# Kernel optimization log

Hardware: AMD Instinct MI355X
Metric: run time of the kernel (lower is better)

The kernel has to match this reference:

```python
import jax, jax.numpy as jnp
import numpy as np

N = 50000      # num_users == num_products (required by the original forward's reuse of edge_index)
E = 800000
F_IN = 128
HID = 256
CLS = 64


def sage_conv(x_src, x_dst, e_src, e_dst, w_l, b_l, w_r, num_dst):
    """PyG SAGEConv (mean aggr, bipartite): lin_l(mean_j x_src[j]) + lin_r(x_dst)."""
    msg = x_src[e_src]                                             # [E, d]
    agg = jax.ops.segment_sum(msg, e_dst, num_segments=num_dst)    # [num_dst, d]
    cnt = jax.ops.segment_sum(jnp.ones((e_dst.shape[0],), x_src.dtype), e_dst,
                              num_segments=num_dst)
    mean = agg / jnp.maximum(cnt, 1.0)[:, None]
    return mean @ w_l.T + b_l + x_dst @ w_r.T


def setup_inputs() -> dict:
    key = jax.random.key(0)
    ks = jax.random.split(key, 16)
    def lin(k, out_d, in_d):
        s = 1.0 / np.sqrt(in_d)
        return jax.random.uniform(k, (out_d, in_d), jnp.float32, -s, s)
    return {
        'x_user': jax.random.normal(ks[0], (N, F_IN), jnp.float32),
        'x_product': jax.random.normal(ks[1], (N, F_IN), jnp.float32),
        'edge_index': jax.random.randint(ks[2], (2, E), 0, N, jnp.int64 if jax.config.jax_enable_x64 else jnp.int32),
        # user_conv1: (F_IN,F_IN)->HID
        'w_u1_l': lin(ks[3], HID, F_IN), 'b_u1': jnp.zeros((HID,), jnp.float32), 'w_u1_r': lin(ks[4], HID, F_IN),
        # product_conv1: (F_IN,F_IN)->HID
        'w_p1_l': lin(ks[5], HID, F_IN), 'b_p1': jnp.zeros((HID,), jnp.float32), 'w_p1_r': lin(ks[6], HID, F_IN),
        # user_conv2: (HID,HID)->CLS
        'w_u2_l': lin(ks[7], CLS, HID), 'b_u2': jnp.zeros((CLS,), jnp.float32), 'w_u2_r': lin(ks[8], CLS, HID),
        # product_conv2: (HID,HID)->CLS
        'w_p2_l': lin(ks[9], CLS, HID), 'b_p2': jnp.zeros((CLS,), jnp.float32), 'w_p2_r': lin(ks[10], CLS, HID),
    }


def reference(x_user, x_product, edge_index,
              w_u1_l, b_u1, w_u1_r, w_p1_l, b_p1, w_p1_r,
              w_u2_l, b_u2, w_u2_r, w_p2_l, b_p2, w_p2_r):
    u_idx, p_idx = edge_index[0], edge_index[1]
    # layer 1 (eval mode: dropout is identity)
    x_user_1 = jax.nn.relu(sage_conv(x_user, x_product, u_idx, p_idx,
                                     w_u1_l, b_u1, w_u1_r, N))        # [N, HID] (dst=product-sized)
    x_product_1 = jax.nn.relu(sage_conv(x_product, x_user, p_idx, u_idx,
                                        w_p1_l, b_p1, w_p1_r, N))     # [N, HID]
    # layer 2 (same edge_index reuse as the original code)
    x_user_2 = sage_conv(x_user_1, x_product_1, u_idx, p_idx,
                         w_u2_l, b_u2, w_u2_r, N)                     # [N, CLS]
    x_product_2 = sage_conv(x_product_1, x_user_1, p_idx, u_idx,
                            w_p2_l, b_p2, w_p2_r, N)                  # [N, CLS]
    return x_user_2, x_product_2
```

## Files before the change

### kernel.cpp

```cpp
#include <hip/hip_runtime.h>
#include <stdint.h>

#define Nn 50000
#define Ee 800000
#define FIN 128
#define HIDD 256
#define CLSS 64

#define NBIN 98
#define BSH 9
#define BINSZ 512
#define BCAP 16384
#define EPB 2048
#define NEB ((Ee + EPB - 1) / EPB)

#define MT_TOT 782
#define GX 112

typedef unsigned int uint_t;
typedef unsigned short us_t;
typedef __attribute__((ext_vector_type(8))) short short8;
typedef __attribute__((ext_vector_type(4))) float f32x4;
typedef __attribute__((ext_vector_type(2))) float f32x2;

__device__ inline float bflo(uint_t v) { union { uint_t u; float f; } c; c.u = v << 16; return c.f; }
__device__ inline float bfhi(uint_t v) { union { uint_t u; float f; } c; c.u = v & 0xffff0000u; return c.f; }
__device__ inline us_t f2bf(float f) {
    union { float f; uint_t u; } c; c.f = f;
    uint_t u = c.u;
    u += 0x7fffu + ((u >> 16) & 1u);
    return (us_t)(u >> 16);
}

#define GLOAD(gp, lp)                                                      \
    __builtin_amdgcn_global_load_lds(                                      \
        (const __attribute__((address_space(1))) unsigned int*)(gp),       \
        (__attribute__((address_space(3))) unsigned int*)(lp), 16, 0, 0)

__global__ __launch_bounds__(512) void k_front(
    const int* __restrict__ ei,
    const float* __restrict__ xu, const float* __restrict__ xp,
    const float* __restrict__ w1, const float* __restrict__ w2,
    const float* __restrict__ w3, const float* __restrict__ w4,
    const float* __restrict__ w5, const float* __restrict__ w6,
    const float* __restrict__ w7, const float* __restrict__ w8,
    us_t* __restrict__ cu, us_t* __restrict__ cp,
    uint_t* __restrict__ f8u, uint_t* __restrict__ f8p,
    us_t* __restrict__ wc10, us_t* __restrict__ wc11,
    us_t* __restrict__ wc20, us_t* __restrict__ wc21,
    int* __restrict__ bin_cnt,
    uint_t* __restrict__ ent_p, uint_t* __restrict__ ent_u) {
    __shared__ int hist[2 * NBIN];
    __shared__ int base[2 * NBIN];
    int bx = blockIdx.x, tid = threadIdx.x;

    if (bx < NEB) {
        int e0 = bx * EPB;
        int n = Ee - e0; if (n > EPB) n = EPB;
        for (int i = tid; i < 2 * NBIN; i += 512) hist[i] = 0;
        __syncthreads();
        for (int i = tid; i < n; i += 512) {
            int u = ei[e0 + i], p = ei[Ee + e0 + i];
            atomicAdd(&hist[p >> BSH], 1);
            atomicAdd(&hist[NBIN + (u >> BSH)], 1);
        }
        __syncthreads();
        for (int i = tid; i < 2 * NBIN; i += 512) {
            int c = hist[i];
            base[i] = c ? atomicAdd(&bin_cnt[i], c) : 0;
        }
        __syncthreads();
        for (int i = tid; i < 2 * NBIN; i += 512) hist[i] = base[i];
        __syncthreads();
        for (int i = tid; i < n; i += 512) {
            int u = ei[e0 + i], p = ei[Ee + e0 + i];
            int bp = p >> BSH, bu = u >> BSH;
            int rp = atomicAdd(&hist[bp], 1);
            if (rp < BCAP)
                ent_p[(size_t)bp * BCAP + rp] = ((uint_t)(p & (BINSZ - 1)) << 16) | (uint_t)u;
            int ru = atomicAdd(&hist[NBIN + bu], 1);
            if (ru < BCAP)
                ent_u[(size_t)bu * BCAP + ru] = ((uint_t)(u & (BINSZ - 1)) << 16) | (uint_t)p;
        }
    } else if (bx < NEB + 96) {
        int i = (bx - NEB) * 512 + tid;
        const float* wp; us_t* dst;
        if (i < 32768) {
            int seg = i >> 13; int loc = i & 8191;
            int row = loc >> 5, col = (loc & 31) * 4;
            switch (seg) {
                case 0: wp = w1; dst = wc10 + (size_t)row * 256 + col; break;
                case 1: wp = w2; dst = wc10 + (size_t)row * 256 + 128 + col; break;
                case 2: wp = w3; dst = wc11 + (size_t)row * 256 + col; break;
                default: wp = w4; dst = wc11 + (size_t)row * 256 + 128 + col; break;
            }
            float4 v = reinterpret_cast<const float4*>(wp)[i & 8191];
            ushort4 o;
            o.x = f2bf(v.x); o.y = f2bf(v.y); o.z = f2bf(v.z); o.w = f2bf(v.w);
            *reinterpret_cast<ushort4*>(dst) = o;
        } else {
            int j = i - 32768;
            int seg = j >> 12; int loc = j & 4095;
            switch (seg) {
                case 0: wp = w5; dst = wc20; break;
                case 1: wp = w6; dst = wc21 + 64 * 256; break;
                case 2: wp = w7; dst = wc21; break;
                default: wp = w8; dst = wc20 + 64 * 256; break;
            }
            float4 v = reinterpret_cast<const float4*>(wp)[loc];
            ushort4 o;
            o.x = f2bf(v.x); o.y = f2bf(v.y); o.z = f2bf(v.z); o.w = f2bf(v.w);
            reinterpret_cast<ushort4*>(dst)[loc] = o;
        }
    } else {
        int bcx = bx - NEB - 96;
        int side = bcx & 1;
        const float* in = side ? xp : xu;
        us_t* comb = side ? cu : cp;
        uint_t* o8 = side ? f8p : f8u;
        const int n4 = (Nn * FIN) / 4;
        int i = (bcx >> 1) * 512 + tid;
        int stride = 256 * 512;
        for (; i < n4; i += stride) {
            float4 v = reinterpret_cast<const float4*>(in)[i];
            ushort4 o;
            o.x = f2bf(v.x); o.y = f2bf(v.y); o.z = f2bf(v.z); o.w = f2bf(v.w);
            int node = i >> 5;
            int col = (i & 31) * 4;
            *reinterpret_cast<ushort4*>(comb + (size_t)node * 256 + 128 + col) = o;
            int pk = __builtin_amdgcn_cvt_pk_fp8_f32(v.x, v.y, 0, false);
            pk = __builtin_amdgcn_cvt_pk_fp8_f32(v.z, v.w, pk, true);
            o8[i] = (uint_t)pk;
        }
    }
}

__global__ __launch_bounds__(512) void k_scatter(
    const uint_t* __restrict__ ent_p, const uint_t* __restrict__ ent_u,
    const int* __restrict__ bin_cnt,
    int* __restrict__ off, int* __restrict__ cnt,
    int* __restrict__ src_p, int* __restrict__ src_u) {
    __shared__ int ca[BINSZ];
    __shared__ int cb[BINSZ];
    __shared__ int bb[128];
    int side = blockIdx.y, b = blockIdx.x, t = threadIdx.x;
    const uint_t* E = (side ? ent_u : ent_p) + (size_t)b * BCAP;
    int* src = side ? src_u : src_p;

    if (t < 128) {
        int v = 0;
        if (t < NBIN) { v = bin_cnt[side * NBIN + t]; if (v > BCAP) v = BCAP; }
        bb[t] = v;
    }
    __syncthreads();
    #pragma unroll
    for (int d = 1; d < 128; d <<= 1) {
        int x = 0;
        if (t < 128 && t >= d) x = bb[t - d];
        __syncthreads();
        if (t < 128) bb[t] += x;
        __syncthreads();
    }
    int nb = bin_cnt[side * NBIN + b]; if (nb > BCAP) nb = BCAP;
    int base = bb[b] - nb;

    ca[t] = 0;
    __syncthreads();
    for (int i = t; i < nb; i += 512)
        atomicAdd(&ca[E[i] >> 16], 1);
    __syncthreads();
    int v = ca[t];
    int* A = ca; int* B = cb;
    #pragma unroll
    for (int d = 1; d < BINSZ; d <<= 1) {
        int x = A[t] + ((t >= d) ? A[t - d] : 0);
        B[t] = x;
        __syncthreads();
        int* tmp = A; A = B; B = tmp;
    }
    int excl = A[t] - v;
    B[t] = excl;
    __syncthreads();
    for (int i = t; i < nb; i += 512) {
        uint_t e = E[i];
        int sl = atomicAdd(&B[e >> 16], 1);
        src[base + sl] = (int)(e & 0xffffu);
    }
    int d = (b << BSH) + t;
    if (d < Nn) {
        off[side * Nn + d] = base + excl;
        cnt[side * Nn + d] = v;
    }
}

__global__ __launch_bounds__(256) void k_agg1(
    const uint4* __restrict__ xu8, const uint4* __restrict__ xp8,
    const int* __restrict__ off, const int* __restrict__ cnt,
    const int* __restrict__ src_p, const int* __restrict__ src_u,
    us_t* __restrict__ cu, us_t* __restrict__ cp) {
    int side = blockIdx.y;
    const uint4* X = side ? xp8 : xu8;
    const int* of = off + side * Nn;
    const int* cn = cnt + side * Nn;
    const int* sr = side ? src_u : src_p;
    us_t* out = side ? cp : cu;

    int node = blockIdx.x * 32 + (threadIdx.x >> 3);
    if (node >= Nn) return;
    int l = threadIdx.x & 7;
    int s = of[node], c = cn[node];
    float ac[16];
    #pragma unroll
    for (int i = 0; i < 16; ++i) ac[i] = 0.f;

    int j = 0;
    for (; j + 8 <= c; j += 8) {
        int ss[8];
        #pragma unroll
        for (int q = 0; q < 8; ++q) ss[q] = sr[s + j + q];
        uint4 vv[8];
        #pragma unroll
        for (int q = 0; q < 8; ++q) vv[q] = X[(size_t)ss[q] * 8 + l];
        #pragma unroll
        for (int q = 0; q < 8; ++q) {
            const uint_t* pw = reinterpret_cast<const uint_t*>(&vv[q]);
            #pragma unroll
            for (int h = 0; h < 4; ++h) {
                f32x2 plo = __builtin_amdgcn_cvt_pk_f32_fp8((int)pw[h], false);
                f32x2 phi = __builtin_amdgcn_cvt_pk_f32_fp8((int)pw[h], true);
                ac[h * 4 + 0] += plo[0]; ac[h * 4 + 1] += plo[1];
                ac[h * 4 + 2] += phi[0]; ac[h * 4 + 3] += phi[1];
            }
        }
    }
    for (; j < c; ++j) {
        uint4 v0 = X[(size_t)sr[s + j] * 8 + l];
        const uint_t* pw = reinterpret_cast<const uint_t*>(&v0);
        #pragma unroll
        for (int h = 0; h < 4; ++h) {
            f32x2 plo = __builtin_amdgcn_cvt_pk_f32_fp8((int)pw[h], false);
            f32x2 phi = __builtin_amdgcn_cvt_pk_f32_fp8((int)pw[h], true);
            ac[h * 4 + 0] += plo[0]; ac[h * 4 + 1] += plo[1];
            ac[h * 4 + 2] += phi[0]; ac[h * 4 + 3] += phi[1];
        }
    }
    float inv = 1.0f / fmaxf((float)c, 1.0f);
    uint_t ow[8];
    #pragma unroll
    for (int i = 0; i < 8; ++i)
        ow[i] = (uint_t)f2bf(ac[2 * i] * inv) | ((uint_t)f2bf(ac[2 * i + 1] * inv) << 16);
    uint4* dst = reinterpret_cast<uint4*>(out + (size_t)node * 256 + l * 16);
    uint4 o0 = {ow[0], ow[1], ow[2], ow[3]};
    uint4 o1 = {ow[4], ow[5], ow[6], ow[7]};
    dst[0] = o0;
    dst[1] = o1;
}

__global__ __launch_bounds__(256) void k_agg2(
    const uint4* __restrict__ tu, const uint4* __restrict__ tp,
    const int* __restrict__ off, const int* __restrict__ cnt,
    const int* __restrict__ src_p, const int* __restrict__ src_u,
    float* __restrict__ ou, float* __restrict__ op) {
    int side = blockIdx.y;
    const uint4* T = side ? tp : tu;
    const int* of = off + side * Nn;
    const int* cn = cnt + side * Nn;
    const int* sr = side ? src_u : src_p;
    float* out = side ? op : ou;

    int node = blockIdx.x * 32 + (threadIdx.x >> 3);
    if (node >= Nn) return;
    int l = threadIdx.x & 7;
    int s = of[node], c = cn[node];
    float ac[8];
    #pragma unroll
    for (int i = 0; i < 8; ++i) ac[i] = 0.f;

    int j = 0;
    for (; j + 8 <= c; j += 8) {
        int ss[8];
        #pragma unroll
        for (int q = 0; q < 8; ++q) ss[q] = sr[s + j + q];
        uint4 vv[8];
        #pragma unroll
        for (int q = 0; q < 8; ++q) vv[q] = T[(size_t)ss[q] * 8 + l];
        #pragma unroll
        for (int q = 0; q < 8; ++q) {
            const uint_t* pw = reinterpret_cast<const uint_t*>(&vv[q]);
            #pragma unroll
            for (int h = 0; h < 4; ++h) {
                ac[h * 2 + 0] += bflo(pw[h]);
                ac[h * 2 + 1] += bfhi(pw[h]);
            }
        }
    }
    for (; j < c; ++j) {
        uint4 v0 = T[(size_t)sr[s + j] * 8 + l];
        const uint_t* pw = reinterpret_cast<const uint_t*>(&v0);
        #pragma unroll
        for (int h = 0; h < 4; ++h) {
            ac[h * 2 + 0] += bflo(pw[h]);
            ac[h * 2 + 1] += bfhi(pw[h]);
        }
    }
    float inv = 1.0f / fmaxf((float)c, 1.0f);
    float4* po = reinterpret_cast<float4*>(out + (size_t)node * 64) + l * 2;
    float4 p0 = po[0], p1 = po[1];
    p0.x += ac[0] * inv; p0.y += ac[1] * inv; p0.z += ac[2] * inv; p0.w += ac[3] * inv;
    p1.x += ac[4] * inv; p1.y += ac[5] * inv; p1.z += ac[6] * inv; p1.w += ac[7] * inv;
    po[0] = p0; po[1] = p1;
}

#define STAGE_A(Ag, mt, b)                                                          \
    {                                                                               \
        int base_ = (mt) * 64;                                                      \
        _Pragma("unroll")                                                           \
        for (int ii = 0; ii < 4; ++ii) {                                            \
            int s_ = ii * 512 + tid;                                                \
            int row_ = s_ >> 5, ks_ = s_ & 31;                                      \
            int ksl_ = ks_ ^ (row_ & 7);                                            \
            int gr_ = base_ + row_; if (gr_ >= Nn) gr_ = Nn - 1;                    \
            GLOAD((Ag) + (size_t)gr_ * 256 + ksl_ * 8, &sA[b][(s_ - lane) * 8]);    \
        }                                                                           \
    }

__global__ __launch_bounds__(512) void k_mm1(
    const us_t* __restrict__ cu, const us_t* __restrict__ cp,
    const us_t* __restrict__ wc10, const us_t* __restrict__ wc11,
    const float* __restrict__ bu1, const float* __restrict__ bp1,
    us_t* __restrict__ hu, us_t* __restrict__ hp) {
    __shared__ us_t sA[2][64 * 256];
    int tid = threadIdx.x, lane = tid & 63;
    int wv = tid >> 6, wr = wv >> 2, wc = wv & 3;
    int job = blockIdx.y;
    const us_t* Ag = job ? cp : cu;
    const us_t* W = job ? wc11 : wc10;
    const float* bias = job ? bp1 : bu1;
    us_t* C = job ? hp : hu;

    short8 wf[4][8];
    #pragma unroll
    for (int n = 0; n < 4; ++n)
        #pragma unroll
        for (int ks = 0; ks < 8; ++ks) {
            int col = wc * 64 + n * 16 + (lane & 15);
            wf[n][ks] = *reinterpret_cast<const short8*>(
                W + (size_t)col * 256 + ks * 32 + (lane >> 4) * 8);
        }
    float bv[4];
    #pragma unroll
    for (int n = 0; n < 4; ++n) bv[n] = bias[wc * 64 + n * 16 + (lane & 15)];

    int bx = blockIdx.x;
    int NT = (MT_TOT - 1 - bx) / GX + 1;
    STAGE_A(Ag, bx, 0);
    for (int t = 0; t < NT; ++t) {
        int mt = bx + t * GX;
        if (t + 1 < NT) {
            STAGE_A(Ag, bx + (t + 1) * GX, (t + 1) & 1);
            asm volatile("s_waitcnt vmcnt(4)" ::: "memory");
        } else {
            asm volatile("s_waitcnt vmcnt(0)" ::: "memory");
        }
        __syncthreads();
        const us_t* sAc = sA[t & 1];

        f32x4 acc[2][4];
        #pragma unroll
        for (int m = 0; m < 2; ++m)
            #pragma unroll
            for (int n = 0; n < 4; ++n)
                #pragma unroll
                for (int i = 0; i < 4; ++i) acc[m][n][i] = 0.f;

        #pragma unroll
        for (int ks = 0; ks < 8; ++ks) {
            short8 af[2];
            #pragma unroll
            for (int m = 0; m < 2; ++m) {
                int row = wr * 32 + m * 16 + (lane & 15);
                int sl = (ks * 4 + (lane >> 4)) ^ (row & 7);
                af[m] = *reinterpret_cast<const short8*>(&sAc[row * 256 + sl * 8]);
            }
            #pragma unroll
            for (int m = 0; m < 2; ++m)
                #pragma unroll
                for (int n = 0; n < 4; ++n)
                    acc[m][n] = __builtin_amdgcn_mfma_f32_16x16x32_bf16(
                        af[m], wf[n][ks], acc[m][n], 0, 0, 0);
        }

        int mbase = mt * 64;
        #pragma unroll
        for (int n = 0; n < 4; ++n) {
            int col = wc * 64 + n * 16 + (lane & 15);
            #pragma unroll
            for (int m = 0; m < 2; ++m) {
                int row0 = mbase + wr * 32 + m * 16 + ((lane >> 4) << 2);
                #pragma unroll
                for (int j = 0; j < 4; ++j) {
                    int row = row0 + j;
                    if (row < Nn)
                        C[(size_t)row * HIDD + col] =
                            f2bf(fmaxf(acc[m][n][j] + bv[n], 0.f));
                }
            }
        }
        __syncthreads();
    }
}

__global__ __launch_bounds__(512) void k_mm2(
    const us_t* __restrict__ hu, const us_t* __restrict__ hp,
    const us_t* __restrict__ wc20, const us_t* __restrict__ wc21,
    const float* __restrict__ bu2, const float* __restrict__ bp2,
    us_t* __restrict__ tu, us_t* __restrict__ tp,
    float* __restrict__ ou, float* __restrict__ op) {
    __shared__ us_t sA[2][64 * 256];
    int tid = threadIdx.x, lane = tid & 63;
    int wv = tid >> 6, wr = wv >> 2, wc = wv & 3;
    int job = blockIdx.y;
    const us_t* Ag = job ? hp : hu;
    const us_t* W = job ? wc21 : wc20;
    const float* bias = job ? bu2 : bp2;
    us_t* T = job ? tp : tu;
    float* O = job ? ou : op;

    short8 wf[2][8];
    #pragma unroll
    for (int n = 0; n < 2; ++n)
        #pragma unroll
        for (int ks = 0; ks < 8; ++ks) {
            int col = wc * 32 + n * 16 + (lane & 15);
            wf[n][ks] = *reinterpret_cast<const short8*>(
                W + (size_t)col * 256 + ks * 32 + (lane >> 4) * 8);
        }
    float bv[2];
    #pragma unroll
    for (int n = 0; n < 2; ++n) {
        int col = wc * 32 + n * 16 + (lane & 15);
        bv[n] = (col >= 64) ? bias[col - 64] : 0.f;
    }

    int bx = blockIdx.x;
    int NT = (MT_TOT - 1 - bx) / GX + 1;
    STAGE_A(Ag, bx, 0);
    for (int t = 0; t < NT; ++t) {
        int mt = bx + t * GX;
        if (t + 1 < NT) {
            STAGE_A(Ag, bx + (t + 1) * GX, (t + 1) & 1);
            asm volatile("s_waitcnt vmcnt(4)" ::: "memory");
        } else {
            asm volatile("s_waitcnt vmcnt(0)" ::: "memory");
        }
        __syncthreads();
        const us_t* sAc = sA[t & 1];

        f32x4 acc[2][2];
        #pragma unroll
        for (int m = 0; m < 2; ++m)
            #pragma unroll
            for (int n = 0; n < 2; ++n)
                #pragma unroll
                for (int i = 0; i < 4; ++i) acc[m][n][i] = 0.f;

        #pragma unroll
        for (int ks = 0; ks < 8; ++ks) {
            short8 af[2];
            #pragma unroll
            for (int m = 0; m < 2; ++m) {
                int row = wr * 32 + m * 16 + (lane & 15);
                int sl = (ks * 4 + (lane >> 4)) ^ (row & 7);
                af[m] = *reinterpret_cast<const short8*>(&sAc[row * 256 + sl * 8]);
            }
            #pragma unroll
            for (int m = 0; m < 2; ++m)
                #pragma unroll
                for (int n = 0; n < 2; ++n)
                    acc[m][n] = __builtin_amdgcn_mfma_f32_16x16x32_bf16(
                        af[m], wf[n][ks], acc[m][n], 0, 0, 0);
        }

        int mbase = mt * 64;
        #pragma unroll
        for (int n = 0; n < 2; ++n) {
            int col = wc * 32 + n * 16 + (lane & 15);
            bool top = col < 64;
            int cc = top ? col : col - 64;
            #pragma unroll
            for (int m = 0; m < 2; ++m) {
                int row0 = mbase + wr * 32 + m * 16 + ((lane >> 4) << 2);
                #pragma unroll
                for (int j = 0; j < 4; ++j) {
                    int row = row0 + j;
                    if (row >= Nn) continue;
                    float v = acc[m][n][j] + bv[n];
                    if (top) T[(size_t)row * 64 + cc] = f2bf(v);
                    else     O[(size_t)row * 64 + cc] = v;
                }
            }
        }
        __syncthreads();
    }
}

extern "C" void kernel_launch(void* const* d_in, const int* in_sizes, int n_in,
                              void* d_out, int out_size, void* d_ws, size_t ws_size,
                              hipStream_t stream) {
    const float* x_user    = (const float*)d_in[0];
    const float* x_product = (const float*)d_in[1];
    const int*   ei        = (const int*)d_in[2];
    const float* w_u1_l = (const float*)d_in[3];
    const float* b_u1   = (const float*)d_in[4];
    const float* w_u1_r = (const float*)d_in[5];
    const float* w_p1_l = (const float*)d_in[6];
    const float* b_p1   = (const float*)d_in[7];
    const float* w_p1_r = (const float*)d_in[8];
    const float* w_u2_l = (const float*)d_in[9];
    const float* b_u2   = (const float*)d_in[10];
    const float* w_u2_r = (const float*)d_in[11];
    const float* w_p2_l = (const float*)d_in[12];
    const float* b_p2   = (const float*)d_in[13];
    const float* w_p2_r = (const float*)d_in[14];

    float* out_u = (float*)d_out;
    float* out_p = out_u + (size_t)Nn * CLSS;

    char* w = (char*)d_ws;
    int* bin_cnt  = (int*)w; w += (size_t)2 * NBIN * 4;
    int* off  = (int*)w;  w += (size_t)2 * Nn * 4;
    int* cnt  = (int*)w;  w += (size_t)2 * Nn * 4;
    int* src_p = (int*)w; w += (size_t)Ee * 4;
    int* src_u = (int*)w; w += (size_t)Ee * 4;
    uint_t* ent_p = (uint_t*)w; w += (size_t)NBIN * BCAP * 4;
    uint_t* ent_u = (uint_t*)w; w += (size_t)NBIN * BCAP * 4;
    uintptr_t a = (uintptr_t)w; a = (a + 255) & ~(uintptr_t)255; w = (char*)a;
    us_t* cu   = (us_t*)w; w += (size_t)Nn * 256 * 2;
    us_t* cp   = (us_t*)w; w += (size_t)Nn * 256 * 2;
    uint_t* xf8u = (uint_t*)w; w += (size_t)Nn * FIN;
    uint_t* xf8p = (uint_t*)w; w += (size_t)Nn * FIN;
    us_t* h_u  = (us_t*)w; w += (size_t)Nn * HIDD * 2;
    us_t* h_p  = (us_t*)w; w += (size_t)Nn * HIDD * 2;
    us_t* tbuf_u = (us_t*)w; w += (size_t)Nn * CLSS * 2;
    us_t* tbuf_p = (us_t*)w; w += (size_t)Nn * CLSS * 2;
    us_t* wc10 = (us_t*)w; w += (size_t)256 * 256 * 2;
    us_t* wc11 = (us_t*)w; w += (size_t)256 * 256 * 2;
    us_t* wc20 = (us_t*)w; w += (size_t)128 * 256 * 2;
    us_t* wc21 = (us_t*)w; w += (size_t)128 * 256 * 2;

    hipMemsetAsync(bin_cnt, 0, (size_t)2 * NBIN * 4, stream);
    k_front<<<NEB + 96 + 512, 512, 0, stream>>>(
        ei, x_user, x_product,
        w_u1_l, w_u1_r, w_p1_l, w_p1_r, w_u2_l, w_u2_r, w_p2_l, w_p2_r,
        cu, cp, xf8u, xf8p, wc10, wc11, wc20, wc21,
        bin_cnt, ent_p, ent_u);
    dim3 gsc(NBIN, 2);
    k_scatter<<<gsc, 512, 0, stream>>>(ent_p, ent_u, bin_cnt,
                                       off, cnt, src_p, src_u);

    dim3 ga1((Nn + 31) / 32, 2);
    k_agg1<<<ga1, 256, 0, stream>>>((const uint4*)xf8u, (const uint4*)xf8p,
                                    off, cnt, src_p, src_u, cu, cp);
    dim3 g1(GX, 2);
    k_mm1<<<g1, 512, 0, stream>>>(cu, cp, wc10, wc11, b_u1, b_p1, h_u, h_p);

    dim3 g2(GX, 2);
    k_mm2<<<g2, 512, 0, stream>>>(h_u, h_p, wc20, wc21, b_u2, b_p2,
                                  tbuf_u, tbuf_p, out_u, out_p);
    dim3 ga2((Nn + 31) / 32, 2);
    k_agg2<<<ga2, 256, 0, stream>>>((const uint4*)tbuf_u, (const uint4*)tbuf_p,
                                    off, cnt, src_p, src_u, out_u, out_p);
}
```

Baseline: 183.0 us.

## Fuse layer-1 and layer-2 GEMMs into one kernel keeping hidden tile in LDS

Merges k_mm1 and k_mm2 into a single kernel, k_mmf. Each 64-row hidden tile is written to padded shared memory instead of global memory, and the second GEMM reads it from there. This removes the global write and re-read of the two Nn x 256 bf16 hidden buffers and one kernel launch. In exchange it raises register pressure, since both weight fragment sets are held in registers, raises LDS use, and adds a barrier between the two phases.

Measured after the change: 179.8 us. Within noise of the previous version (-1.7%).

```diff
diff --git a/kernel.cpp b/kernel.cpp
--- a/kernel.cpp
+++ b/kernel.cpp
@@ -16,6 +16,8 @@
 
 #define MT_TOT 782
 #define GX 112
+
+#define SHP 264
 
 typedef unsigned int uint_t;
 typedef unsigned short us_t;
@@ -324,32 +326,55 @@
         }                                                                           \
     }
 
-__global__ __launch_bounds__(512) void k_mm1(
+__global__ __launch_bounds__(512) void k_mmf(
     const us_t* __restrict__ cu, const us_t* __restrict__ cp,
     const us_t* __restrict__ wc10, const us_t* __restrict__ wc11,
+    const us_t* __restrict__ wc20, const us_t* __restrict__ wc21,
     const float* __restrict__ bu1, const float* __restrict__ bp1,
-    us_t* __restrict__ hu, us_t* __restrict__ hp) {
+    const float* __restrict__ bu2, const float* __restrict__ bp2,
+    us_t* __restrict__ tu, us_t* __restrict__ tp,
+    float* __restrict__ ou, float* __restrict__ op) {
     __shared__ us_t sA[2][64 * 256];
+    __shared__ us_t sH[64 * SHP];
     int tid = threadIdx.x, lane = tid & 63;
     int wv = tid >> 6, wr = wv >> 2, wc = wv & 3;
     int job = blockIdx.y;
     const us_t* Ag = job ? cp : cu;
-    const us_t* W = job ? wc11 : wc10;
-    const float* bias = job ? bp1 : bu1;
-    us_t* C = job ? hp : hu;
-
-    short8 wf[4][8];
+    const us_t* W1 = job ? wc11 : wc10;
+    const us_t* W2 = job ? wc21 : wc20;
+    const float* b1 = job ? bp1 : bu1;
+    const float* b2 = job ? bu2 : bp2;
+    us_t* T = job ? tp : tu;
+    float* O = job ? ou : op;
+
+    short8 wf1[4][8];
     #pragma unroll
     for (int n = 0; n < 4; ++n)
         #pragma unroll
         for (int ks = 0; ks < 8; ++ks) {
             int col = wc * 64 + n * 16 + (lane & 15);
-            wf[n][ks] = *reinterpret_cast<const short8*>(
-                W + (size_t)col * 256 + ks * 32 + (lane >> 4) * 8);
-        }
-    float bv[4];
-    #pragma unroll
-    for (int n = 0; n < 4; ++n) bv[n] = bias[wc * 64 + n * 16 + (lane & 15)];
+            wf1[n][ks] = *reinterpret_cast<const short8*>(
+                W1 + (size_t)col * 256 + ks * 32 + (lane >> 4) * 8);
+        }
+    float bv1[4];
+    #pragma unroll
+    for (int n = 0; n < 4; ++n) bv1[n] = b1[wc * 64 + n * 16 + (lane & 15)];
+
+    short8 wf2[2][8];
+    #pragma unroll
+    for (int n = 0; n < 2; ++n)
+        #pragma unroll
+        for (int ks = 0; ks < 8; ++ks) {
+            int col = wc * 32 + n * 16 + (lane & 15);
+            wf2[n][ks] = *reinterpret_cast<const short8*>(
+                W2 + (size_t)col * 256 + ks * 32 + (lane >> 4) * 8);
+        }
+    float bv2[2];
+    #pragma unroll
+    for (int n = 0; n < 2; ++n) {
+        int col = wc * 32 + n * 16 + (lane & 15);
+        bv2[n] = (col >= 64) ? b2[col - 64] : 0.f;
+    }
 
     int bx = blockIdx.x;
     int NT = (MT_TOT - 1 - bx) / GX + 1;
@@ -365,13 +390,13 @@
         __syncthreads();
         const us_t* sAc = sA[t & 1];
 
-        f32x4 acc[2][4];
+        f32x4 acc1[2][4];
         #pragma unroll
         for (int m = 0; m < 2; ++m)
             #pragma unroll
             for (int n = 0; n < 4; ++n)
                 #pragma unroll
-                for (int i = 0; i < 4; ++i) acc[m][n][i] = 0.f;
+                for (int i = 0; i < 4; ++i) acc1[m][n][i] = 0.f;
 
         #pragma unroll
         for (int ks = 0; ks < 8; ++ks) {
@@ -386,99 +411,47 @@
             for (int m = 0; m < 2; ++m)
                 #pragma unroll
                 for (int n = 0; n < 4; ++n)
-                    acc[m][n] = __builtin_amdgcn_mfma_f32_16x16x32_bf16(
-                        af[m], wf[n][ks], acc[m][n], 0, 0, 0);
-        }
-
-        int mbase = mt * 64;
+                    acc1[m][n] = __builtin_amdgcn_mfma_f32_16x16x32_bf16(
+                        af[m], wf1[n][ks], acc1[m][n], 0, 0, 0);
+        }
+
         #pragma unroll
         for (int n = 0; n < 4; ++n) {
             int col = wc * 64 + n * 16 + (lane & 15);
             #pragma unroll
             for (int m = 0; m < 2; ++m) {
-                int row0 = mbase + wr * 32 + m * 16 + ((lane >> 4) << 2);
+                int r0 = wr * 32 + m * 16 + ((lane >> 4) << 2);
                 #pragma unroll
-                for (int j = 0; j < 4; ++j) {
-                    int row = row0 + j;
-                    if (row < Nn)
-                        C[(size_t)row * HIDD + col] =
-                            f2bf(fmaxf(acc[m][n][j] + bv[n], 0.f));
-                }
-            }
-        }
-        __syncthreads();
-    }
-}
-
-__global__ __launch_bounds__(512) void k_mm2(
-    const us_t* __restrict__ hu, const us_t* __restrict__ hp,
-    const us_t* __restrict__ wc20, const us_t* __restrict__ wc21,
-    const float* __restrict__ bu2, const float* __restrict__ bp2,
-    us_t* __restrict__ tu, us_t* __restrict__ tp,
-    float* __restrict__ ou, float* __restrict__ op) {
-    __shared__ us_t sA[2][64 * 256];
-    int tid = threadIdx.x, lane = tid & 63;
-    int wv = tid >> 6, wr = wv >> 2, wc = wv & 3;
-    int job = blockIdx.y;
-    const us_t* Ag = job ? hp : hu;
-    const us_t* W = job ? wc21 : wc20;
-    const float* bias = job ? bu2 : bp2;
-    us_t* T = job ? tp : tu;
-    float* O = job ? ou : op;
-
-    short8 wf[2][8];
-    #pragma unroll
-    for (int n = 0; n < 2; ++n)
-        #pragma unroll
-        for (int ks = 0; ks < 8; ++ks) {
-            int col = wc * 32 + n * 16 + (lane & 15);
-            wf[n][ks] = *reinterpret_cast<const short8*>(
-                W + (size_t)col * 256 + ks * 32 + (lane >> 4) * 8);
-        }
-    float bv[2];
-    #pragma unroll
-    for (int n = 0; n < 2; ++n) {
-        int col = wc * 32 + n * 16 + (lane & 15);
-        bv[n] = (col >= 64) ? bias[col - 64] : 0.f;
-    }
-
-    int bx = blockIdx.x;
-    int NT = (MT_TOT - 1 - bx) / GX + 1;
-    STAGE_A(Ag, bx, 0);
-    for (int t = 0; t < NT; ++t) {
-        int mt = bx + t * GX;
-        if (t + 1 < NT) {
-            STAGE_A(Ag, bx + (t + 1) * GX, (t + 1) & 1);
-            asm volatile("s_waitcnt vmcnt(4)" ::: "memory");
-        } else {
-            asm volatile("s_waitcnt vmcnt(0)" ::: "memory");
-        }
-        __syncthreads();
-        const us_t* sAc = sA[t & 1];
-
-        f32x4 acc[2][2];
+                for (int j = 0; j < 4; ++j)
+                    sH[(r0 + j) * SHP + col] =
+                        f2bf(fmaxf(acc1[m][n][j] + bv1[n], 0.f));
+            }
+        }
+        __syncthreads();
+
+        f32x4 acc2[2][2];
         #pragma unroll
         for (int m = 0; m < 2; ++m)
             #pragma unroll
             for (int n = 0; n < 2; ++n)
                 #pragma unroll
-                for (int i = 0; i < 4; ++i) acc[m][n][i] = 0.f;
+                for (int i = 0; i < 4; ++i) acc2[m][n][i] = 0.f;
 
         #pragma unroll
         for (int ks = 0; ks < 8; ++ks) {
-            short8 af[2];
+            short8 af2[2];
             #pragma unroll
             for (int m = 0; m < 2; ++m) {
                 int row = wr * 32 + m * 16 + (lane & 15);
-                int sl = (ks * 4 + (lane >> 4)) ^ (row & 7);
-                af[m] = *reinterpret_cast<const short8*>(&sAc[row * 256 + sl * 8]);
+                af2[m] = *reinterpret_cast<const short8*>(
+                    &sH[row * SHP + ks * 32 + (lane >> 4) * 8]);
             }
             #pragma unroll
             for (int m = 0; m < 2; ++m)
                 #pragma unroll
                 for (int n = 0; n < 2; ++n)
-                    acc[m][n] = __builtin_amdgcn_mfma_f32_16x16x32_bf16(
-                        af[m], wf[n][ks], acc[m][n], 0, 0, 0);
+                    acc2[m][n] = __builtin_amdgcn_mfma_f32_16x16x32_bf16(
+                        af2[m], wf2[n][ks], acc2[m][n], 0, 0, 0);
         }
 
         int mbase = mt * 64;
@@ -494,13 +467,12 @@
                 for (int j = 0; j < 4; ++j) {
                     int row = row0 + j;
                     if (row >= Nn) continue;
-                    float v = acc[m][n][j] + bv[n];
+                    float v = acc2[m][n][j] + bv2[n];
                     if (top) T[(size_t)row * 64 + cc] = f2bf(v);
                     else     O[(size_t)row * 64 + cc] = v;
                 }
             }
         }
-        __syncthreads();
     }
 }
 
@@ -539,8 +511,6 @@
     us_t* cp   = (us_t*)w; w += (size_t)Nn * 256 * 2;
     uint_t* xf8u = (uint_t*)w; w += (size_t)Nn * FIN;
     uint_t* xf8p = (uint_t*)w; w += (size_t)Nn * FIN;
-    us_t* h_u  = (us_t*)w; w += (size_t)Nn * HIDD * 2;
-    us_t* h_p  = (us_t*)w; w += (size_t)Nn * HIDD * 2;
     us_t* tbuf_u = (us_t*)w; w += (size_t)Nn * CLSS * 2;
     us_t* tbuf_p = (us_t*)w; w += (size_t)Nn * CLSS * 2;
     us_t* wc10 = (us_t*)w; w += (size_t)256 * 256 * 2;
@@ -561,12 +531,12 @@
     dim3 ga1((Nn + 31) / 32, 2);
     k_agg1<<<ga1, 256, 0, stream>>>((const uint4*)xf8u, (const uint4*)xf8p,
                                     off, cnt, src_p, src_u, cu, cp);
+
     dim3 g1(GX, 2);
-    k_mm1<<<g1, 512, 0, stream>>>(cu, cp, wc10, wc11, b_u1, b_p1, h_u, h_p);
-
-    dim3 g2(GX, 2);
-    k_mm2<<<g2, 512, 0, stream>>>(h_u, h_p, wc20, wc21, b_u2, b_p2,
+    k_mmf<<<g1, 512, 0, stream>>>(cu, cp, wc10, wc11, wc20, wc21,
+                                  b_u1, b_p1, b_u2, b_p2,
                                   tbuf_u, tbuf_p, out_u, out_p);
+
     dim3 ga2((Nn + 31) / 32, 2);
     k_agg2<<<ga2, 256, 0, stream>>>((const uint4*)tbuf_u, (const uint4*)tbuf_p,
                                     off, cnt, src_p, src_u, out_u, out_p);
```
